# Kernel tuning notes

Measured on AMD Instinct MI355X. Metric: run time of the kernel, lower is better.

The kernel has to match this reference:

```python
import jax, jax.numpy as jnp
import numpy as np

H = 10  # hidden size per direction
I = 1   # input size


def _lstm_scan(x_tbi, Wih, Whh, bih, bhh):
    """Single-direction LSTM over time-major input x_tbi: [T, B, I] -> [T, B, H].
    PyTorch gate order: i, f, g, o."""
    T, B, _ = x_tbi.shape
    # Precompute input contribution for all timesteps: [T, B, 4H]
    pre = jnp.einsum('tbi,gi->tbg', x_tbi, Wih) + bih + bhh

    def step(carry, p):
        h, c = carry
        gates = p + h @ Whh.T  # [B, 4H]
        i, f, g, o = jnp.split(gates, 4, axis=-1)
        i = jax.nn.sigmoid(i)
        f = jax.nn.sigmoid(f)
        g = jnp.tanh(g)
        o = jax.nn.sigmoid(o)
        c = f * c + i * g
        h = o * jnp.tanh(c)
        return (h, c), h

    h0 = jnp.zeros((B, H), x_tbi.dtype)
    (_, _), hs = jax.lax.scan(step, (h0, h0), pre)
    return hs  # [T, B, H]


def setup_inputs() -> dict:
    key = jax.random.key(0)
    ks = jax.random.split(key, 12)
    B, T = 256, 4096
    s = 1.0 / np.sqrt(H)  # PyTorch LSTM init range
    u = lambda k, shape: jax.random.uniform(k, shape, jnp.float32, -s, s)
    inp = {
        'data': jax.random.normal(ks[0], (B, T, I), jnp.float32),
        # forward direction
        'Wih_f': u(ks[1], (4 * H, I)),
        'Whh_f': u(ks[2], (4 * H, H)),
        'bih_f': u(ks[3], (4 * H,)),
        'bhh_f': u(ks[4], (4 * H,)),
        # backward direction
        'Wih_b': u(ks[5], (4 * H, I)),
        'Whh_b': u(ks[6], (4 * H, H)),
        'bih_b': u(ks[7], (4 * H,)),
        'bhh_b': u(ks[8], (4 * H,)),
        # final linear (kaiming_uniform fan_in=20 -> bound sqrt(6/20))
        'Wout': jax.random.uniform(ks[9], (1, 2 * H), jnp.float32, -np.sqrt(6.0 / (2 * H)), np.sqrt(6.0 / (2 * H))),
        'bout': jax.random.uniform(ks[10], (1,), jnp.float32, -1.0 / np.sqrt(2 * H), 1.0 / np.sqrt(2 * H)),
    }
    return inp


def reference(data, Wih_f, Whh_f, bih_f, bhh_f, Wih_b, Whh_b, bih_b, bhh_b, Wout, bout):
    # data: [B, T, 1] (batch_first) -> time-major [T, B, 1]
    x = jnp.transpose(data, (1, 0, 2))
    hf = _lstm_scan(x, Wih_f, Whh_f, bih_f, bhh_f)                 # [T, B, H]
    hb = _lstm_scan(x[::-1], Wih_b, Whh_b, bih_b, bhh_b)[::-1]     # [T, B, H]
    h = jnp.concatenate([hf, hb], axis=-1)                          # [T, B, 2H]
    y = h @ Wout.T + bout                                           # [T, B, 1]
    return jnp.transpose(y, (1, 0, 2))                              # [B, T, 1]
```

## Files before the change

### kernel.cpp

```cpp
#include <hip/hip_runtime.h>

#define T_LEN 4096
#define B_N   256
#define SEG_N 16
#define OWN   256
#define WARM  128
#define SMAX  (OWN + WARM)
#define YSTR  (SMAX + 2)
#define L2E   1.4426950408889634f

typedef float v2f __attribute__((ext_vector_type(2)));

__device__ __forceinline__ v2f pk_mul(v2f a, v2f b) {
    v2f d; asm("v_pk_mul_f32 %0, %1, %2" : "=v"(d) : "v"(a), "v"(b)); return d;
}
__device__ __forceinline__ v2f pk_fma(v2f a, v2f b, v2f c) {
    v2f d; asm("v_pk_fma_f32 %0, %1, %2, %3" : "=v"(d) : "v"(a), "v"(b), "v"(c)); return d;
}
__device__ __forceinline__ v2f pk_add(v2f a, v2f b) {
    v2f d; asm("v_pk_add_f32 %0, %1, %2" : "=v"(d) : "v"(a), "v"(b)); return d;
}

__global__ __launch_bounds__(64) void Model_82008105550530_kernel(
    const float* __restrict__ data,
    const float* __restrict__ Wih_f, const float* __restrict__ Whh_f,
    const float* __restrict__ bih_f, const float* __restrict__ bhh_f,
    const float* __restrict__ Wih_b, const float* __restrict__ Whh_b,
    const float* __restrict__ bih_b, const float* __restrict__ bhh_b,
    const float* __restrict__ Wout, const float* __restrict__ bout,
    float* __restrict__ out)
{
    __shared__ v2f   hbuf[72];
    __shared__ float ylds[4 * YSTR + 64];

    const int l   = threadIdx.x;
    const int grp = blockIdx.x >> 6;
    const int dir = grp >> 4;
    const int seg = grp & 15;
    const int b0  = (blockIdx.x & 63) << 2;

    const bool gate = (l < 40);
    const int  c    = gate ? (l / 10) : ((l < 44) ? (l - 40) : 0);
    const int  u    = gate ? (l % 10) : 0;

    const float* Whh = dir ? Whh_b : Whh_f;
    const float* Wih = dir ? Wih_b : Wih_f;
    const float* bi  = dir ? bih_b : bih_f;
    const float* bh  = dir ? bhh_b : bhh_f;

    v2f Wif[10], Wgo[10];
    float wih_i, wih_f, wih_g, wih_o, b_i, b_f, b_g, b_o;
    if (gate) {
        const int rI = u, rF = 10 + u, rG = 20 + u, rO = 30 + u;
#pragma unroll
        for (int m = 0; m < 10; ++m) {
            Wif[m] = (v2f){-L2E * Whh[rI * 10 + m], -L2E * Whh[rF * 10 + m]};
            Wgo[m] = (v2f){2.0f * L2E * Whh[rG * 10 + m], -L2E * Whh[rO * 10 + m]};
        }
        wih_i = -L2E * Wih[rI];        wih_f = -L2E * Wih[rF];
        wih_g = 2.0f * L2E * Wih[rG];  wih_o = -L2E * Wih[rO];
        b_i = -L2E * (bi[rI] + bh[rI]);       b_f = -L2E * (bi[rF] + bh[rF]);
        b_g = 2.0f * L2E * (bi[rG] + bh[rG]); b_o = -L2E * (bi[rO] + bh[rO]);
    } else {
#pragma unroll
        for (int m = 0; m < 10; ++m) {
            Wif[m] = (v2f){Wout[dir * 10 + m], 0.0f};
            Wgo[m] = (v2f){0.0f, 0.0f};
        }
        wih_i = wih_f = wih_g = wih_o = 0.0f;
        b_i = (dir == 0) ? bout[0] : 0.0f;
        b_f = b_g = b_o = 0.0f;
    }

    const int  hw = gate ? (c * 12 + u) : (48 + (l - 40));
    const bool yw_on = (l >= 40) && (l < 44);
    int        yw  = yw_on ? (c * YSTR) : (4 * YSTR + l);
    const int  ywd = yw_on ? 1 : 0;

    if (l < 48) hbuf[l] = (v2f){0.0f, 0.0f};

    const int wpre  = (dir == 0) ? ((seg == 0) ? 0 : WARM)
                                 : ((seg == SEG_N - 1) ? 0 : WARM);
    const int steps = OWN + wpre;

    const float* xrow = data + (size_t)(b0 + c) * T_LEN;
    const float* px = (dir == 0) ? (xrow + seg * OWN - wpre)
                                 : (xrow + seg * OWN + OWN - 1 + wpre - 7);
    const int pstep = (dir == 0) ? 8 : -8;

    float4 A  = *(const float4*)px;
    float4 Bv = *(const float4*)(px + 4);

    float C = 0.0f;
    const v2f* hb = &hbuf[c * 12];

#define STEP(XV)                                                              \
    {                                                                         \
        const v2f h0 = hb[0], h1 = hb[1], h2 = hb[2], h3 = hb[3], h4 = hb[4], \
                  h5 = hb[5], h6 = hb[6], h7 = hb[7], h8 = hb[8], h9 = hb[9]; \
        v2f s0 = pk_mul(Wif[0], h0);                                          \
        s0 = pk_fma(Wif[1], h1, s0); s0 = pk_fma(Wif[2], h2, s0);             \
        s0 = pk_fma(Wif[3], h3, s0); s0 = pk_fma(Wif[4], h4, s0);             \
        v2f s1 = pk_mul(Wif[5], h5);                                          \
        s1 = pk_fma(Wif[6], h6, s1); s1 = pk_fma(Wif[7], h7, s1);             \
        s1 = pk_fma(Wif[8], h8, s1); s1 = pk_fma(Wif[9], h9, s1);             \
        const v2f aif = pk_add(s0, s1);                                       \
        v2f t0 = pk_mul(Wgo[0], h0);                                          \
        t0 = pk_fma(Wgo[1], h1, t0); t0 = pk_fma(Wgo[2], h2, t0);             \
        t0 = pk_fma(Wgo[3], h3, t0); t0 = pk_fma(Wgo[4], h4, t0);             \
        v2f t1 = pk_mul(Wgo[5], h5);                                          \
        t1 = pk_fma(Wgo[6], h6, t1); t1 = pk_fma(Wgo[7], h7, t1);             \
        t1 = pk_fma(Wgo[8], h8, t1); t1 = pk_fma(Wgo[9], h9, t1);             \
        const v2f ago = pk_add(t0, t1);                                       \
        const float gi = aif.x + fmaf(XV, wih_i, b_i);                        \
        const float gf = aif.y + fmaf(XV, wih_f, b_f);                        \
        const float gg = ago.x + fmaf(XV, wih_g, b_g);                        \
        const float go = ago.y + fmaf(XV, wih_o, b_o);                        \
        ylds[yw] = gi;  yw += ywd;         \
        const float ri = __builtin_amdgcn_rcpf(1.0f + __builtin_amdgcn_exp2f(gi)); \
        const float rf = __builtin_amdgcn_rcpf(1.0f + __builtin_amdgcn_exp2f(gf)); \
        const float rg = __builtin_amdgcn_rcpf(1.0f + __builtin_amdgcn_exp2f(gg)); \
        const float ro = __builtin_amdgcn_rcpf(1.0f + __builtin_amdgcn_exp2f(go)); \
        const float ai = (2.0f * L2E) * ri;         \
        const float ag = fmaf(-2.0f, rg, 1.0f);                  \
        C = fmaf(rf, C, ai * ag);                         \
        const float r2 = __builtin_amdgcn_rcpf(1.0f + __builtin_amdgcn_exp2f(C)); \
        const float mo = -2.0f * ro;                                          \
        const float hn = fmaf(mo, r2, ro);               \
        hbuf[hw] = (v2f){hn, hn};                                             \
    }

    const int nch = steps >> 3;
    for (int it = 0; it < nch; ++it) {
        const float* pn = px + ((it + 1 < nch) ? (it + 1) : it) * pstep;
        float4 An = *(const float4*)pn;
        float4 Bn = *(const float4*)(pn + 4);

        float q0 = A.x, q1 = A.y, q2 = A.z, q3 = A.w,
              q4 = Bv.x, q5 = Bv.y, q6 = Bv.z, q7 = Bv.w;
        if (dir) {
            float t;
            t = q0; q0 = q7; q7 = t;  t = q1; q1 = q6; q6 = t;
            t = q2; q2 = q5; q5 = t;  t = q3; q3 = q4; q4 = t;
        }
        STEP(q0) STEP(q1) STEP(q2) STEP(q3) STEP(q4) STEP(q5) STEP(q6) STEP(q7)
        A = An; Bv = Bn;
    }

    {
        const v2f h0 = hb[0], h1 = hb[1], h2 = hb[2], h3 = hb[3], h4 = hb[4],
                  h5 = hb[5], h6 = hb[6], h7 = hb[7], h8 = hb[8], h9 = hb[9];
        v2f s0 = pk_mul(Wif[0], h0);
        s0 = pk_fma(Wif[1], h1, s0); s0 = pk_fma(Wif[2], h2, s0);
        s0 = pk_fma(Wif[3], h3, s0); s0 = pk_fma(Wif[4], h4, s0);
        v2f s1 = pk_mul(Wif[5], h5);
        s1 = pk_fma(Wif[6], h6, s1); s1 = pk_fma(Wif[7], h7, s1);
        s1 = pk_fma(Wif[8], h8, s1); s1 = pk_fma(Wif[9], h9, s1);
        const v2f aif = pk_add(s0, s1);
        ylds[yw] = aif.x + b_i;
    }

    for (int i = l; i < 4 * OWN; i += 64) {
        const int ci = i >> 8;
        const int io = i & (OWN - 1);
        const int t  = seg * OWN + io;
        const int sp = (dir == 0) ? (wpre + io) : (OWN - 1 + wpre - io);
        atomicAdd(&out[(size_t)(b0 + ci) * T_LEN + t], ylds[ci * YSTR + sp + 1]);
    }
#undef STEP
}

extern "C" void kernel_launch(void* const* d_in, const int* in_sizes, int n_in,
                              void* d_out, int out_size, void* d_ws, size_t ws_size,
                              hipStream_t stream) {
    const float* data  = (const float*)d_in[0];
    const float* Wih_f = (const float*)d_in[1];
    const float* Whh_f = (const float*)d_in[2];
    const float* bih_f = (const float*)d_in[3];
    const float* bhh_f = (const float*)d_in[4];
    const float* Wih_b = (const float*)d_in[5];
    const float* Whh_b = (const float*)d_in[6];
    const float* bih_b = (const float*)d_in[7];
    const float* bhh_b = (const float*)d_in[8];
    const float* Wout  = (const float*)d_in[9];
    const float* bout  = (const float*)d_in[10];
    float* out = (float*)d_out;

    hipMemsetAsync(out, 0, (size_t)out_size * sizeof(float), stream);
    Model_82008105550530_kernel<<<32 * 64, 64, 0, stream>>>(
        data, Wih_f, Whh_f, bih_f, bhh_f, Wih_b, Whh_b, bih_b, bhh_b, Wout, bout, out);
}
```

Measured before the change: 126.5 us.

## Exchange hidden state via DPP row rotations instead of LDS; halve segment count

Each batch row now gets a 16-lane group, one lane per hidden unit. The recurrent matvec gathers the hidden state with DPP row_ror shuffles, so the per-step LDS write and read of h is gone, along with the LDS latency on the serial dependency chain. Segments double in length (8 per direction instead of 16), which halves the grid to 1024 blocks and cuts redundant warm-up steps. The cost is longer serial chains per block, fewer waves to hide latency, and more packed FMAs per step because of zero-padded weights.

```diff
diff --git a/kernel.cpp b/kernel.cpp
--- a/kernel.cpp
+++ b/kernel.cpp
@@ -2,8 +2,8 @@
 
 #define T_LEN 4096
 #define B_N   256
-#define SEG_N 16
-#define OWN   256
+#define SEG_N 8
+#define OWN   512
 #define WARM  128
 #define SMAX  (OWN + WARM)
 #define YSTR  (SMAX + 2)
@@ -17,8 +17,160 @@
 __device__ __forceinline__ v2f pk_fma(v2f a, v2f b, v2f c) {
     v2f d; asm("v_pk_fma_f32 %0, %1, %2, %3" : "=v"(d) : "v"(a), "v"(b), "v"(c)); return d;
 }
-__device__ __forceinline__ v2f pk_add(v2f a, v2f b) {
-    v2f d; asm("v_pk_add_f32 %0, %1, %2" : "=v"(d) : "v"(a), "v"(b)); return d;
+
+template <int S>
+__device__ __forceinline__ float ror16(float v) {
+    if constexpr (S == 0) return v;
+    else return __int_as_float(__builtin_amdgcn_update_dpp(
+        0, __float_as_int(v), 0x120 | S, 0xF, 0xF, true));
+}
+
+template <int DIR>
+__device__ __forceinline__ void scan_dir(
+    const float* __restrict__ data,
+    const float* __restrict__ Wih, const float* __restrict__ Whh,
+    const float* __restrict__ bih, const float* __restrict__ bhh,
+    const float* __restrict__ Wout, const float* __restrict__ bout,
+    float* __restrict__ out, float* __restrict__ ylds, int seg, int b0)
+{
+    const int l = threadIdx.x;
+    const int c = l >> 4;
+    const int u = l & 15;
+
+    v2f WI[8], WF[8], WG[8], WO[8];
+    v2f WX_if = {0.f, 0.f}, WX_go = {0.f, 0.f};
+    v2f B_if  = {0.f, 0.f}, B_go  = {0.f, 0.f};
+
+    if (u < 10) {
+        const int rI = u, rF = 10 + u, rG = 20 + u, rO = 30 + u;
+#pragma unroll
+        for (int s = 0; s < 8; ++s) {
+            const int mA = (u - s) & 15, mB = (u - s - 8) & 15;
+            const float aI = (mA < 10) ? -L2E * Whh[rI * 10 + mA] : 0.f;
+            const float bI = (mB < 10) ? -L2E * Whh[rI * 10 + mB] : 0.f;
+            const float aF = (mA < 10) ? -L2E * Whh[rF * 10 + mA] : 0.f;
+            const float bF = (mB < 10) ? -L2E * Whh[rF * 10 + mB] : 0.f;
+            const float aG = (mA < 10) ? 2.f * L2E * Whh[rG * 10 + mA] : 0.f;
+            const float bG = (mB < 10) ? 2.f * L2E * Whh[rG * 10 + mB] : 0.f;
+            const float aO = (mA < 10) ? -L2E * Whh[rO * 10 + mA] : 0.f;
+            const float bO = (mB < 10) ? -L2E * Whh[rO * 10 + mB] : 0.f;
+            WI[s] = (v2f){aI, bI}; WF[s] = (v2f){aF, bF};
+            WG[s] = (v2f){aG, bG}; WO[s] = (v2f){aO, bO};
+        }
+        WX_if = (v2f){-L2E * Wih[rI], -L2E * Wih[rF]};
+        WX_go = (v2f){2.f * L2E * Wih[rG], -L2E * Wih[rO]};
+        B_if = (v2f){-L2E * (bih[rI] + bhh[rI]), -L2E * (bih[rF] + bhh[rF])};
+        B_go = (v2f){2.f * L2E * (bih[rG] + bhh[rG]), -L2E * (bih[rO] + bhh[rO])};
+    } else if (u == 10) {
+#pragma unroll
+        for (int s = 0; s < 8; ++s) {
+            const int mA = (u - s) & 15, mB = (u - s - 8) & 15;
+            WI[s] = (v2f){(mA < 10) ? Wout[DIR * 10 + mA] : 0.f,
+                          (mB < 10) ? Wout[DIR * 10 + mB] : 0.f};
+            WF[s] = (v2f){0.f, 0.f}; WG[s] = (v2f){0.f, 0.f}; WO[s] = (v2f){0.f, 0.f};
+        }
+        B_if = (v2f){(DIR == 0) ? bout[0] : 0.f, 0.f};
+    } else {
+#pragma unroll
+        for (int s = 0; s < 8; ++s) {
+            WI[s] = (v2f){0.f, 0.f}; WF[s] = (v2f){0.f, 0.f};
+            WG[s] = (v2f){0.f, 0.f}; WO[s] = (v2f){0.f, 0.f};
+        }
+    }
+
+    const int wpre  = (DIR == 0) ? ((seg == 0) ? 0 : WARM)
+                                 : ((seg == SEG_N - 1) ? 0 : WARM);
+    const int steps = OWN + wpre;
+    const int t0 = seg * OWN - wpre;
+    const int t1 = seg * OWN + OWN - 1 + wpre;
+
+    int yi = (u == 10) ? (c * YSTR) : (4 * YSTR + l);
+    const int ywd = (u == 10) ? 1 : 0;
+
+    float h = 0.0f, C = 0.0f;
+
+    const float* xrow = data + (size_t)(b0 + c) * T_LEN;
+    const float* px = (DIR == 0) ? (xrow + t0) : (xrow + t1 - 7);
+    const int pstep = (DIR == 0) ? 8 : -8;
+    float4 A  = *(const float4*)px;
+    float4 Bv = *(const float4*)(px + 4);
+
+#define H2BUILD                                                               \
+    v2f h2[8];                                                                \
+    h2[0] = (v2f){h,           ror16<8>(h)};                                  \
+    h2[1] = (v2f){ror16<1>(h), ror16<9>(h)};                                  \
+    h2[2] = (v2f){ror16<2>(h), ror16<10>(h)};                                 \
+    h2[3] = (v2f){ror16<3>(h), ror16<11>(h)};                                 \
+    h2[4] = (v2f){ror16<4>(h), ror16<12>(h)};                                 \
+    h2[5] = (v2f){ror16<5>(h), ror16<13>(h)};                                 \
+    h2[6] = (v2f){ror16<6>(h), ror16<14>(h)};                                 \
+    h2[7] = (v2f){ror16<7>(h), ror16<15>(h)};
+
+#define STEP(XV)                                                              \
+    {                                                                         \
+        const v2f X2 = {XV, XV};                                              \
+        const v2f pif = pk_fma(X2, WX_if, B_if);                              \
+        const v2f pgo = pk_fma(X2, WX_go, B_go);                              \
+        H2BUILD                                                               \
+        v2f ai = pk_mul(h2[0], WI[0]);                                        \
+        v2f af = pk_mul(h2[0], WF[0]);                                        \
+        v2f ag = pk_mul(h2[0], WG[0]);                                        \
+        v2f ao = pk_mul(h2[0], WO[0]);                                        \
+        _Pragma("unroll")                                                     \
+        for (int s = 1; s < 8; ++s) {                                         \
+            ai = pk_fma(h2[s], WI[s], ai);                                    \
+            af = pk_fma(h2[s], WF[s], af);                                    \
+            ag = pk_fma(h2[s], WG[s], ag);                                    \
+            ao = pk_fma(h2[s], WO[s], ao);                                    \
+        }                                                                     \
+        const float gi = (ai.x + ai.y) + pif.x;                               \
+        const float gf = (af.x + af.y) + pif.y;                               \
+        const float gg = (ag.x + ag.y) + pgo.x;                               \
+        const float go_ = (ao.x + ao.y) + pgo.y;                              \
+        ylds[yi] = gi;  yi += ywd;         \
+        const float ri = __builtin_amdgcn_rcpf(1.f + __builtin_amdgcn_exp2f(gi)); \
+        const float rf = __builtin_amdgcn_rcpf(1.f + __builtin_amdgcn_exp2f(gf)); \
+        const float rg = __builtin_amdgcn_rcpf(1.f + __builtin_amdgcn_exp2f(gg)); \
+        const float ro = __builtin_amdgcn_rcpf(1.f + __builtin_amdgcn_exp2f(go_)); \
+        const float aiv = (2.f * L2E) * ri;                                   \
+        const float agv = fmaf(-2.f, rg, 1.f);                                \
+        C = fmaf(rf, C, aiv * agv);                       \
+        const float r2 = __builtin_amdgcn_rcpf(1.f + __builtin_amdgcn_exp2f(C)); \
+        const float mo = -2.f * ro;                                           \
+        h = fmaf(mo, r2, ro);                            \
+    }
+
+    const int nch = steps >> 3;
+    for (int it = 0; it < nch; ++it) {
+        const float* pn = px + ((it + 1 < nch) ? (it + 1) : it) * pstep;
+        float4 An = *(const float4*)pn;
+        float4 Bn = *(const float4*)(pn + 4);
+        const float xs[8] = {A.x, A.y, A.z, A.w, Bv.x, Bv.y, Bv.z, Bv.w};
+#pragma unroll
+        for (int r = 0; r < 8; ++r) {
+            const float xv = xs[(DIR == 0) ? r : (7 - r)];
+            STEP(xv)
+        }
+        A = An; Bv = Bn;
+    }
+
+    {
+        H2BUILD
+        v2f ai = pk_mul(h2[0], WI[0]);
+#pragma unroll
+        for (int s = 1; s < 8; ++s) ai = pk_fma(h2[s], WI[s], ai);
+        ylds[yi] = (ai.x + ai.y) + B_if.x;
+    }
+
+    for (int i = l; i < 4 * OWN; i += 64) {
+        const int ci = i >> 9;
+        const int io = i & (OWN - 1);
+        const int t  = seg * OWN + io;
+        const int sp = (DIR == 0) ? (wpre + io) : (OWN - 1 + wpre - io);
+        atomicAdd(&out[(size_t)(b0 + ci) * T_LEN + t], ylds[ci * YSTR + sp + 1]);
+    }
+#undef STEP
+#undef H2BUILD
 }
 
 __global__ __launch_bounds__(64) void Model_82008105550530_kernel(
@@ -30,144 +182,14 @@
     const float* __restrict__ Wout, const float* __restrict__ bout,
     float* __restrict__ out)
 {
-    __shared__ v2f   hbuf[72];
     __shared__ float ylds[4 * YSTR + 64];
-
-    const int l   = threadIdx.x;
+    const int b0  = (blockIdx.x & 63) << 2;
     const int grp = blockIdx.x >> 6;
-    const int dir = grp >> 4;
-    const int seg = grp & 15;
-    const int b0  = (blockIdx.x & 63) << 2;
-
-    const bool gate = (l < 40);
-    const int  c    = gate ? (l / 10) : ((l < 44) ? (l - 40) : 0);
-    const int  u    = gate ? (l % 10) : 0;
-
-    const float* Whh = dir ? Whh_b : Whh_f;
-    const float* Wih = dir ? Wih_b : Wih_f;
-    const float* bi  = dir ? bih_b : bih_f;
-    const float* bh  = dir ? bhh_b : bhh_f;
-
-    v2f Wif[10], Wgo[10];
-    float wih_i, wih_f, wih_g, wih_o, b_i, b_f, b_g, b_o;
-    if (gate) {
-        const int rI = u, rF = 10 + u, rG = 20 + u, rO = 30 + u;
-#pragma unroll
-        for (int m = 0; m < 10; ++m) {
-            Wif[m] = (v2f){-L2E * Whh[rI * 10 + m], -L2E * Whh[rF * 10 + m]};
-            Wgo[m] = (v2f){2.0f * L2E * Whh[rG * 10 + m], -L2E * Whh[rO * 10 + m]};
-        }
-        wih_i = -L2E * Wih[rI];        wih_f = -L2E * Wih[rF];
-        wih_g = 2.0f * L2E * Wih[rG];  wih_o = -L2E * Wih[rO];
-        b_i = -L2E * (bi[rI] + bh[rI]);       b_f = -L2E * (bi[rF] + bh[rF]);
-        b_g = 2.0f * L2E * (bi[rG] + bh[rG]); b_o = -L2E * (bi[rO] + bh[rO]);
-    } else {
-#pragma unroll
-        for (int m = 0; m < 10; ++m) {
-            Wif[m] = (v2f){Wout[dir * 10 + m], 0.0f};
-            Wgo[m] = (v2f){0.0f, 0.0f};
-        }
-        wih_i = wih_f = wih_g = wih_o = 0.0f;
-        b_i = (dir == 0) ? bout[0] : 0.0f;
-        b_f = b_g = b_o = 0.0f;
-    }
-
-    const int  hw = gate ? (c * 12 + u) : (48 + (l - 40));
-    const bool yw_on = (l >= 40) && (l < 44);
-    int        yw  = yw_on ? (c * YSTR) : (4 * YSTR + l);
-    const int  ywd = yw_on ? 1 : 0;
-
-    if (l < 48) hbuf[l] = (v2f){0.0f, 0.0f};
-
-    const int wpre  = (dir == 0) ? ((seg == 0) ? 0 : WARM)
-                                 : ((seg == SEG_N - 1) ? 0 : WARM);
-    const int steps = OWN + wpre;
-
-    const float* xrow = data + (size_t)(b0 + c) * T_LEN;
-    const float* px = (dir == 0) ? (xrow + seg * OWN - wpre)
-                                 : (xrow + seg * OWN + OWN - 1 + wpre - 7);
-    const int pstep = (dir == 0) ? 8 : -8;
-
-    float4 A  = *(const float4*)px;
-    float4 Bv = *(const float4*)(px + 4);
-
-    float C = 0.0f;
-    const v2f* hb = &hbuf[c * 12];
-
-#define STEP(XV)                                                              \
-    {                                                                         \
-        const v2f h0 = hb[0], h1 = hb[1], h2 = hb[2], h3 = hb[3], h4 = hb[4], \
-                  h5 = hb[5], h6 = hb[6], h7 = hb[7], h8 = hb[8], h9 = hb[9]; \
-        v2f s0 = pk_mul(Wif[0], h0);                                          \
-        s0 = pk_fma(Wif[1], h1, s0); s0 = pk_fma(Wif[2], h2, s0);             \
-        s0 = pk_fma(Wif[3], h3, s0); s0 = pk_fma(Wif[4], h4, s0);             \
-        v2f s1 = pk_mul(Wif[5], h5);                                          \
-        s1 = pk_fma(Wif[6], h6, s1); s1 = pk_fma(Wif[7], h7, s1);             \
-        s1 = pk_fma(Wif[8], h8, s1); s1 = pk_fma(Wif[9], h9, s1);             \
-        const v2f aif = pk_add(s0, s1);                                       \
-        v2f t0 = pk_mul(Wgo[0], h0);                                          \
-        t0 = pk_fma(Wgo[1], h1, t0); t0 = pk_fma(Wgo[2], h2, t0);             \
-        t0 = pk_fma(Wgo[3], h3, t0); t0 = pk_fma(Wgo[4], h4, t0);             \
-        v2f t1 = pk_mul(Wgo[5], h5);                                          \
-        t1 = pk_fma(Wgo[6], h6, t1); t1 = pk_fma(Wgo[7], h7, t1);             \
-        t1 = pk_fma(Wgo[8], h8, t1); t1 = pk_fma(Wgo[9], h9, t1);             \
-        const v2f ago = pk_add(t0, t1);                                       \
-        const float gi = aif.x + fmaf(XV, wih_i, b_i);                        \
-        const float gf = aif.y + fmaf(XV, wih_f, b_f);                        \
-        const float gg = ago.x + fmaf(XV, wih_g, b_g);                        \
-        const float go = ago.y + fmaf(XV, wih_o, b_o);                        \
-        ylds[yw] = gi;  yw += ywd;         \
-        const float ri = __builtin_amdgcn_rcpf(1.0f + __builtin_amdgcn_exp2f(gi)); \
-        const float rf = __builtin_amdgcn_rcpf(1.0f + __builtin_amdgcn_exp2f(gf)); \
-        const float rg = __builtin_amdgcn_rcpf(1.0f + __builtin_amdgcn_exp2f(gg)); \
-        const float ro = __builtin_amdgcn_rcpf(1.0f + __builtin_amdgcn_exp2f(go)); \
-        const float ai = (2.0f * L2E) * ri;         \
-        const float ag = fmaf(-2.0f, rg, 1.0f);                  \
-        C = fmaf(rf, C, ai * ag);                         \
-        const float r2 = __builtin_amdgcn_rcpf(1.0f + __builtin_amdgcn_exp2f(C)); \
-        const float mo = -2.0f * ro;                                          \
-        const float hn = fmaf(mo, r2, ro);               \
-        hbuf[hw] = (v2f){hn, hn};                                             \
-    }
-
-    const int nch = steps >> 3;
-    for (int it = 0; it < nch; ++it) {
-        const float* pn = px + ((it + 1 < nch) ? (it + 1) : it) * pstep;
-        float4 An = *(const float4*)pn;
-        float4 Bn = *(const float4*)(pn + 4);
-
-        float q0 = A.x, q1 = A.y, q2 = A.z, q3 = A.w,
-              q4 = Bv.x, q5 = Bv.y, q6 = Bv.z, q7 = Bv.w;
-        if (dir) {
-            float t;
-            t = q0; q0 = q7; q7 = t;  t = q1; q1 = q6; q6 = t;
-            t = q2; q2 = q5; q5 = t;  t = q3; q3 = q4; q4 = t;
-        }
-        STEP(q0) STEP(q1) STEP(q2) STEP(q3) STEP(q4) STEP(q5) STEP(q6) STEP(q7)
-        A = An; Bv = Bn;
-    }
-
-    {
-        const v2f h0 = hb[0], h1 = hb[1], h2 = hb[2], h3 = hb[3], h4 = hb[4],
-                  h5 = hb[5], h6 = hb[6], h7 = hb[7], h8 = hb[8], h9 = hb[9];
-        v2f s0 = pk_mul(Wif[0], h0);
-        s0 = pk_fma(Wif[1], h1, s0); s0 = pk_fma(Wif[2], h2, s0);
-        s0 = pk_fma(Wif[3], h3, s0); s0 = pk_fma(Wif[4], h4, s0);
-        v2f s1 = pk_mul(Wif[5], h5);
-        s1 = pk_fma(Wif[6], h6, s1); s1 = pk_fma(Wif[7], h7, s1);
-        s1 = pk_fma(Wif[8], h8, s1); s1 = pk_fma(Wif[9], h9, s1);
-        const v2f aif = pk_add(s0, s1);
-        ylds[yw] = aif.x + b_i;
-    }
-
-    for (int i = l; i < 4 * OWN; i += 64) {
-        const int ci = i >> 8;
-        const int io = i & (OWN - 1);
-        const int t  = seg * OWN + io;
-        const int sp = (dir == 0) ? (wpre + io) : (OWN - 1 + wpre - io);
-        atomicAdd(&out[(size_t)(b0 + ci) * T_LEN + t], ylds[ci * YSTR + sp + 1]);
-    }
-#undef STEP
+    const int seg = grp & 7;
+    if ((grp >> 3) == 0)
+        scan_dir<0>(data, Wih_f, Whh_f, bih_f, bhh_f, Wout, bout, out, ylds, seg, b0);
+    else
+        scan_dir<1>(data, Wih_b, Whh_b, bih_b, bhh_b, Wout, bout, out, ylds, seg, b0);
 }
 
 extern "C" void kernel_launch(void* const* d_in, const int* in_sizes, int n_in,
@@ -187,6 +209,6 @@
     float* out = (float*)d_out;
 
     hipMemsetAsync(out, 0, (size_t)out_size * sizeof(float), stream);
-    Model_82008105550530_kernel<<<32 * 64, 64, 0, stream>>>(
+    Model_82008105550530_kernel<<<1024, 64, 0, stream>>>(
         data, Wih_f, Whh_f, bih_f, bhh_f, Wih_b, Whh_b, bih_b, bhh_b, Wout, bout, out);
 }
```

New measurement: 136.4 us. 7.8% more time.

## Shorten LSTM segments and map two hidden units per lane across eight batches

Applied to the files above, without the earlier changes.

Halves the owned time segment per block to shorten the serial recurrence chain, and packs eight batch rows per wave with each lane computing two hidden units for all four gates. Hidden-state reads use vectorized float4 LDS loads, and the four gate reciprocals are merged into one rcp using product tricks. This increases warm-up overhead relative to owned work and raises register pressure and per-step arithmetic per lane. The shared reciprocal may lose precision or overflow for large gate products.

```diff
diff --git a/kernel.cpp b/kernel.cpp
--- a/kernel.cpp
+++ b/kernel.cpp
@@ -2,8 +2,8 @@
 
 #define T_LEN 4096
 #define B_N   256
-#define SEG_N 16
-#define OWN   256
+#define SEG_N 32
+#define OWN   128
 #define WARM  128
 #define SMAX  (OWN + WARM)
 #define YSTR  (SMAX + 2)
@@ -11,17 +11,11 @@
 
 typedef float v2f __attribute__((ext_vector_type(2)));
 
-__device__ __forceinline__ v2f pk_mul(v2f a, v2f b) {
-    v2f d; asm("v_pk_mul_f32 %0, %1, %2" : "=v"(d) : "v"(a), "v"(b)); return d;
-}
 __device__ __forceinline__ v2f pk_fma(v2f a, v2f b, v2f c) {
     v2f d; asm("v_pk_fma_f32 %0, %1, %2, %3" : "=v"(d) : "v"(a), "v"(b), "v"(c)); return d;
 }
-__device__ __forceinline__ v2f pk_add(v2f a, v2f b) {
-    v2f d; asm("v_pk_add_f32 %0, %1, %2" : "=v"(d) : "v"(a), "v"(b)); return d;
-}
-
-__global__ __launch_bounds__(64) void Model_82008105550530_kernel(
+
+__global__ __launch_bounds__(64, 2) void Model_82008105550530_kernel(
     const float* __restrict__ data,
     const float* __restrict__ Wih_f, const float* __restrict__ Whh_f,
     const float* __restrict__ bih_f, const float* __restrict__ bhh_f,
@@ -30,54 +24,54 @@
     const float* __restrict__ Wout, const float* __restrict__ bout,
     float* __restrict__ out)
 {
-    __shared__ v2f   hbuf[72];
-    __shared__ float ylds[4 * YSTR + 64];
-
-    const int l   = threadIdx.x;
-    const int grp = blockIdx.x >> 6;
-    const int dir = grp >> 4;
-    const int seg = grp & 15;
-    const int b0  = (blockIdx.x & 63) << 2;
-
-    const bool gate = (l < 40);
-    const int  c    = gate ? (l / 10) : ((l < 44) ? (l - 40) : 0);
-    const int  u    = gate ? (l % 10) : 0;
+    __shared__ __align__(16) v2f hbuf[144];
+    __shared__ float ylds[8 * YSTR + 64];
+
+    const int l = threadIdx.x;
+    const int c = l >> 3;
+    const int p = l & 7;
+
+    const int bid = blockIdx.x;
+    const int dir = bid >> 10;
+    const int seg = (bid >> 5) & 31;
+    const int b0  = (bid & 31) << 3;
 
     const float* Whh = dir ? Whh_b : Whh_f;
     const float* Wih = dir ? Wih_b : Wih_f;
     const float* bi  = dir ? bih_b : bih_f;
     const float* bh  = dir ? bhh_b : bhh_f;
-
-    v2f Wif[10], Wgo[10];
-    float wih_i, wih_f, wih_g, wih_o, b_i, b_f, b_g, b_o;
-    if (gate) {
-        const int rI = u, rF = 10 + u, rG = 20 + u, rO = 30 + u;
-#pragma unroll
-        for (int m = 0; m < 10; ++m) {
-            Wif[m] = (v2f){-L2E * Whh[rI * 10 + m], -L2E * Whh[rF * 10 + m]};
-            Wgo[m] = (v2f){2.0f * L2E * Whh[rG * 10 + m], -L2E * Whh[rO * 10 + m]};
+    const float ybias = (dir == 0) ? bout[0] : 0.0f;
+
+    v2f W2[4][10], wx2[4], bb2[4];
+#pragma unroll
+    for (int g = 0; g < 4; ++g) {
+        wx2[g] = (v2f){0.f, 0.f}; bb2[g] = (v2f){0.f, 0.f};
+#pragma unroll
+        for (int m = 0; m < 10; ++m) W2[g][m] = (v2f){0.f, 0.f};
+    }
+    if (p < 5) {
+#pragma unroll
+        for (int g = 0; g < 4; ++g) {
+            const float sc = (g == 2) ? (2.0f * L2E) : (-L2E);
+            const int rA = g * 10 + 2 * p, rB = rA + 1;
+#pragma unroll
+            for (int m = 0; m < 10; ++m)
+                W2[g][m] = (v2f){sc * Whh[rA * 10 + m], sc * Whh[rB * 10 + m]};
+            wx2[g] = (v2f){sc * Wih[rA], sc * Wih[rB]};
+            bb2[g] = (v2f){sc * (bi[rA] + bh[rA]), sc * (bi[rB] + bh[rB])};
         }
-        wih_i = -L2E * Wih[rI];        wih_f = -L2E * Wih[rF];
-        wih_g = 2.0f * L2E * Wih[rG];  wih_o = -L2E * Wih[rO];
-        b_i = -L2E * (bi[rI] + bh[rI]);       b_f = -L2E * (bi[rF] + bh[rF]);
-        b_g = 2.0f * L2E * (bi[rG] + bh[rG]); b_o = -L2E * (bi[rO] + bh[rO]);
-    } else {
-#pragma unroll
-        for (int m = 0; m < 10; ++m) {
-            Wif[m] = (v2f){Wout[dir * 10 + m], 0.0f};
-            Wgo[m] = (v2f){0.0f, 0.0f};
-        }
-        wih_i = wih_f = wih_g = wih_o = 0.0f;
-        b_i = (dir == 0) ? bout[0] : 0.0f;
-        b_f = b_g = b_o = 0.0f;
-    }
-
-    const int  hw = gate ? (c * 12 + u) : (48 + (l - 40));
-    const bool yw_on = (l >= 40) && (l < 44);
-    int        yw  = yw_on ? (c * YSTR) : (4 * YSTR + l);
-    const int  ywd = yw_on ? 1 : 0;
-
-    if (l < 48) hbuf[l] = (v2f){0.0f, 0.0f};
+    } else if (p == 5) {
+#pragma unroll
+        for (int m = 0; m < 10; ++m) W2[0][m] = (v2f){Wout[dir * 10 + m], 0.f};
+        bb2[0] = (v2f){ybias, 0.f};
+    }
+
+    const int hw1 = (p < 5) ? (c * 12 + 2 * p) : (96 + c * 6 + (p - 5) * 2);
+    const int hw2 = hw1 + 1;
+    int yw = (p == 5) ? (c * YSTR) : (8 * YSTR + l);
+    const int ywd = (p == 5) ? 1 : 0;
+
+    for (int i = l; i < 96; i += 64) hbuf[i] = (v2f){0.f, 0.f};
 
     const int wpre  = (dir == 0) ? ((seg == 0) ? 0 : WARM)
                                  : ((seg == SEG_N - 1) ? 0 : WARM);
@@ -87,47 +81,62 @@
     const float* px = (dir == 0) ? (xrow + seg * OWN - wpre)
                                  : (xrow + seg * OWN + OWN - 1 + wpre - 7);
     const int pstep = (dir == 0) ? 8 : -8;
-
     float4 A  = *(const float4*)px;
     float4 Bv = *(const float4*)(px + 4);
 
-    float C = 0.0f;
-    const v2f* hb = &hbuf[c * 12];
+    float Cx = 0.0f, Cy = 0.0f;
+    const float4* hbF = (const float4*)&hbuf[c * 12];
+
+#define UNIT_TAIL(GI, GF, GG, GO, CREG, HN)                                   \
+    {                                                                         \
+        const float qi = 1.0f + __builtin_amdgcn_exp2f(GI);                   \
+        const float qf = 1.0f + __builtin_amdgcn_exp2f(GF);                   \
+        const float qg = 1.0f + __builtin_amdgcn_exp2f(GG);                   \
+        const float qo = 1.0f + __builtin_amdgcn_exp2f(GO);                   \
+        const float p1 = qi * qf;                                             \
+        const float p2 = p1 * qg;                                             \
+        const float p3 = p2 * qo;                                             \
+        const float R  = __builtin_amdgcn_rcpf(p3);                           \
+        const float ro = p2 * R;                                              \
+        const float R2 = qo * R;                                              \
+        const float rg = p1 * R2;                                             \
+        const float R1 = qg * R2;                                             \
+        const float rf = qi * R1;                                             \
+        const float ri = qf * R1;                                             \
+        const float ai = (2.0f * L2E) * ri;                                   \
+        const float ag = fmaf(-2.0f, rg, 1.0f);                               \
+        CREG = fmaf(rf, CREG, ai * ag);                                       \
+        const float r2 = __builtin_amdgcn_rcpf(                               \
+            1.0f + __builtin_amdgcn_exp2f(CREG));                             \
+        HN = fmaf(-2.0f * ro, r2, ro);                                        \
+    }
 
 #define STEP(XV)                                                              \
     {                                                                         \
-        const v2f h0 = hb[0], h1 = hb[1], h2 = hb[2], h3 = hb[3], h4 = hb[4], \
-                  h5 = hb[5], h6 = hb[6], h7 = hb[7], h8 = hb[8], h9 = hb[9]; \
-        v2f s0 = pk_mul(Wif[0], h0);                                          \
-        s0 = pk_fma(Wif[1], h1, s0); s0 = pk_fma(Wif[2], h2, s0);             \
-        s0 = pk_fma(Wif[3], h3, s0); s0 = pk_fma(Wif[4], h4, s0);             \
-        v2f s1 = pk_mul(Wif[5], h5);                                          \
-        s1 = pk_fma(Wif[6], h6, s1); s1 = pk_fma(Wif[7], h7, s1);             \
-        s1 = pk_fma(Wif[8], h8, s1); s1 = pk_fma(Wif[9], h9, s1);             \
-        const v2f aif = pk_add(s0, s1);                                       \
-        v2f t0 = pk_mul(Wgo[0], h0);                                          \
-        t0 = pk_fma(Wgo[1], h1, t0); t0 = pk_fma(Wgo[2], h2, t0);             \
-        t0 = pk_fma(Wgo[3], h3, t0); t0 = pk_fma(Wgo[4], h4, t0);             \
-        v2f t1 = pk_mul(Wgo[5], h5);                                          \
-        t1 = pk_fma(Wgo[6], h6, t1); t1 = pk_fma(Wgo[7], h7, t1);             \
-        t1 = pk_fma(Wgo[8], h8, t1); t1 = pk_fma(Wgo[9], h9, t1);             \
-        const v2f ago = pk_add(t0, t1);                                       \
-        const float gi = aif.x + fmaf(XV, wih_i, b_i);                        \
-        const float gf = aif.y + fmaf(XV, wih_f, b_f);                        \
-        const float gg = ago.x + fmaf(XV, wih_g, b_g);                        \
-        const float go = ago.y + fmaf(XV, wih_o, b_o);                        \
-        ylds[yw] = gi;  yw += ywd;         \
-        const float ri = __builtin_amdgcn_rcpf(1.0f + __builtin_amdgcn_exp2f(gi)); \
-        const float rf = __builtin_amdgcn_rcpf(1.0f + __builtin_amdgcn_exp2f(gf)); \
-        const float rg = __builtin_amdgcn_rcpf(1.0f + __builtin_amdgcn_exp2f(gg)); \
-        const float ro = __builtin_amdgcn_rcpf(1.0f + __builtin_amdgcn_exp2f(go)); \
-        const float ai = (2.0f * L2E) * ri;         \
-        const float ag = fmaf(-2.0f, rg, 1.0f);                  \
-        C = fmaf(rf, C, ai * ag);                         \
-        const float r2 = __builtin_amdgcn_rcpf(1.0f + __builtin_amdgcn_exp2f(C)); \
-        const float mo = -2.0f * ro;                                          \
-        const float hn = fmaf(mo, r2, ro);               \
-        hbuf[hw] = (v2f){hn, hn};                                             \
+        const v2f X2 = {XV, XV};                                              \
+        v2f A0 = pk_fma(X2, wx2[0], bb2[0]);                                  \
+        v2f A1 = pk_fma(X2, wx2[1], bb2[1]);                                  \
+        v2f A2 = pk_fma(X2, wx2[2], bb2[2]);                                  \
+        v2f A3 = pk_fma(X2, wx2[3], bb2[3]);                                  \
+        const float4 P0 = hbF[0], P1 = hbF[1], P2 = hbF[2], P3 = hbF[3],      \
+                     P4 = hbF[4];                                             \
+        const v2f hp[10] = {{P0.x, P0.y}, {P0.z, P0.w}, {P1.x, P1.y},         \
+                            {P1.z, P1.w}, {P2.x, P2.y}, {P2.z, P2.w},         \
+                            {P3.x, P3.y}, {P3.z, P3.w}, {P4.x, P4.y},         \
+                            {P4.z, P4.w}};                                    \
+        _Pragma("unroll")                                                     \
+        for (int m = 0; m < 10; ++m) {                                        \
+            A0 = pk_fma(W2[0][m], hp[m], A0);                                 \
+            A1 = pk_fma(W2[1][m], hp[m], A1);                                 \
+            A2 = pk_fma(W2[2][m], hp[m], A2);                                 \
+            A3 = pk_fma(W2[3][m], hp[m], A3);                                 \
+        }                                                                     \
+        ylds[yw] = A0.x;  yw += ywd;       \
+        float hnx, hny;                                                       \
+        UNIT_TAIL(A0.x, A1.x, A2.x, A3.x, Cx, hnx)                            \
+        UNIT_TAIL(A0.y, A1.y, A2.y, A3.y, Cy, hny)                            \
+        hbuf[hw1] = (v2f){hnx, hnx};                                          \
+        hbuf[hw2] = (v2f){hny, hny};                                          \
     }
 
     const int nch = steps >> 3;
@@ -148,26 +157,27 @@
     }
 
     {
-        const v2f h0 = hb[0], h1 = hb[1], h2 = hb[2], h3 = hb[3], h4 = hb[4],
-                  h5 = hb[5], h6 = hb[6], h7 = hb[7], h8 = hb[8], h9 = hb[9];
-        v2f s0 = pk_mul(Wif[0], h0);
-        s0 = pk_fma(Wif[1], h1, s0); s0 = pk_fma(Wif[2], h2, s0);
-        s0 = pk_fma(Wif[3], h3, s0); s0 = pk_fma(Wif[4], h4, s0);
-        v2f s1 = pk_mul(Wif[5], h5);
-        s1 = pk_fma(Wif[6], h6, s1); s1 = pk_fma(Wif[7], h7, s1);
-        s1 = pk_fma(Wif[8], h8, s1); s1 = pk_fma(Wif[9], h9, s1);
-        const v2f aif = pk_add(s0, s1);
-        ylds[yw] = aif.x + b_i;
-    }
-
-    for (int i = l; i < 4 * OWN; i += 64) {
-        const int ci = i >> 8;
+        v2f A0 = bb2[0];
+        const float4 P0 = hbF[0], P1 = hbF[1], P2 = hbF[2], P3 = hbF[3],
+                     P4 = hbF[4];
+        const v2f hp[10] = {{P0.x, P0.y}, {P0.z, P0.w}, {P1.x, P1.y},
+                            {P1.z, P1.w}, {P2.x, P2.y}, {P2.z, P2.w},
+                            {P3.x, P3.y}, {P3.z, P3.w}, {P4.x, P4.y},
+                            {P4.z, P4.w}};
+#pragma unroll
+        for (int m = 0; m < 10; ++m) A0 = pk_fma(W2[0][m], hp[m], A0);
+        ylds[yw] = A0.x;
+    }
+
+    for (int i = l; i < 8 * OWN; i += 64) {
+        const int ci = i >> 7;
         const int io = i & (OWN - 1);
         const int t  = seg * OWN + io;
         const int sp = (dir == 0) ? (wpre + io) : (OWN - 1 + wpre - io);
         atomicAdd(&out[(size_t)(b0 + ci) * T_LEN + t], ylds[ci * YSTR + sp + 1]);
     }
 #undef STEP
+#undef UNIT_TAIL
 }
 
 extern "C" void kernel_launch(void* const* d_in, const int* in_sizes, int n_in,
@@ -187,6 +197,6 @@
     float* out = (float*)d_out;
 
     hipMemsetAsync(out, 0, (size_t)out_size * sizeof(float), stream);
-    Model_82008105550530_kernel<<<32 * 64, 64, 0, stream>>>(
+    Model_82008105550530_kernel<<<2048, 64, 0, stream>>>(
         data, Wih_f, Whh_f, bih_f, bhh_f, Wih_b, Whh_b, bih_b, bhh_b, Wout, bout, out);
 }
```

After: 134.5 us. +6.3%, slower.
